# Optimization experiments

Hardware: AMD Instinct MI355X
Metric: run time of the kernel (lower is better)

## Reference

```python
import jax, jax.numpy as jnp
import numpy as np
import math
from itertools import combinations_with_replacement

# ---- module constants (init: d_key=16, d_val=64, p=2, is_causal=True) ----
D_KEY, D_VAL, P = 16, 64, 2
B, H, N = 1, 8, 4096

# M: multisets of size p over d_key indices -> [m, p], m = comb(d_key+p-1, p) = 136
M_NP = np.array(list(combinations_with_replacement(range(D_KEY), P)), dtype=np.int64)

def _n_multiset_perms(row):
    counts = np.bincount(row, minlength=D_KEY)
    denom = 1
    for c in counts:
        denom *= math.factorial(int(c))
    return math.factorial(P) / denom

C_NP = np.array([_n_multiset_perms(r) for r in M_NP], dtype=np.float32)  # [m]
ALPHA = np.float32(1.0 / (math.factorial(P) * D_KEY ** (P / 2)))
M_J = jnp.asarray(M_NP)
C_J = jnp.asarray(C_NP)


def _phi(x):
    # x: [..., d_key] -> polynomial features [..., m] via gather + product over p indices
    return jnp.prod(x[..., M_J], axis=-1)


def setup_inputs() -> dict:
    key = jax.random.key(0)
    kq, kk, kv = jax.random.split(key, 3)
    Q = jax.random.normal(kq, (B, H, N, D_KEY), dtype=jnp.float32)
    K = jax.random.normal(kk, (B, H, N, D_KEY), dtype=jnp.float32)
    V = jax.random.normal(kv, (B, H, N, D_VAL), dtype=jnp.float32)
    return {"Q": Q, "K": K, "V": V, "continue_prev": 0}


def reference(Q, K, V, continue_prev):
    # continue_prev is False (0): fresh sequence, no carried state.
    Phi_Q = _phi(Q)  # [b,h,n,m]
    Phi_K = _phi(K)  # [b,h,n,m]
    # causal accumulation: cumsum over token axis (-3)
    H_S = jnp.cumsum(Phi_K[..., None] * V[..., None, :], axis=-3) * ALPHA  # [b,h,n,m,d_val]
    H_Z = jnp.cumsum(Phi_K[..., None], axis=-3) * ALPHA                    # [b,h,n,m,1]
    S_term = jnp.einsum('m,bhnm,bhnmd->bhnd', C_J, Phi_Q, H_S)  # [b,h,n,d_val]
    Z_term = jnp.einsum('m,bhnm,bhnmd->bhnd', C_J, Phi_Q, H_Z)  # [b,h,n,1]
    return (S_term, Z_term)
```

## Files before the change

### kernel.cpp

```cpp
#include <hip/hip_runtime.h>


#define SEQN 4096
#define NHEAD 8
#define DKEY 16
#define DVAL 64
#define CHUNK 128
#define NCHUNK 32
#define ALPHA 0.03125f

typedef float f32x4 __attribute__((ext_vector_type(4)));
typedef __bf16 bf16x4 __attribute__((ext_vector_type(4)));
typedef __bf16 bf16x8 __attribute__((ext_vector_type(8)));
typedef unsigned long long u64;
typedef u64 u64x2 __attribute__((ext_vector_type(2)));

#define SW512(row, colb) (((row) << 9) + ((colb) ^ (((row) & 7) << 4)))
#define SW256(row, colb) (((row) << 8) + ((colb) ^ (((row) & 7) << 4)))

__device__ inline float bf2f(__bf16 x) {
    unsigned short u = __builtin_bit_cast(unsigned short, x);
    unsigned int v = ((unsigned int)u) << 16;
    return __builtin_bit_cast(float, v);
}

__global__ __launch_bounds__(512, 1)
void p01_state(const float* __restrict__ Kg, const float* __restrict__ Vg,
               const float* __restrict__ Qg, __bf16* __restrict__ G,
               float* __restrict__ Og)
{
    __shared__ __align__(128) unsigned char Vt2[80 * 256];
    __shared__ __align__(128) unsigned char Ktf[16 * 512];
    __shared__ __align__(128) unsigned char Kl[128 * 32];
    const int tid = threadIdx.x;
    const int w = tid >> 6;
    const int lane = tid & 63;
    const int r = lane & 15, g = lane >> 4;
    const int bid = blockIdx.x;
    const int h = bid & 7, c = bid >> 3;
    const int k0 = c * CHUNK;
    const int qb = k0 + 16 * w;

    float qr[16];
    {
        const float* qp = Qg + ((size_t)h * SEQN + qb + r) * DKEY;
        #pragma unroll
        for (int m = 0; m < 4; ++m) {
            const f32x4 v = *(const f32x4*)(qp + 4 * m);
            qr[4 * m + 0] = v[0]; qr[4 * m + 1] = v[1];
            qr[4 * m + 2] = v[2]; qr[4 * m + 3] = v[3];
        }
    }

    {
        const int key = tid >> 2, part = tid & 3;
        const float* kp = Kg + ((size_t)h * SEQN + k0 + key) * DKEY + 4 * part;
        const f32x4 a = *(const f32x4*)kp;
        #pragma unroll
        for (int j = 0; j < 4; ++j)
            *(float*)(Ktf + SW512(4 * part + j, key * 4)) = a[j];
        bf16x4 o;
        #pragma unroll
        for (int j = 0; j < 4; ++j) o[j] = (__bf16)a[j];
        *(bf16x4*)(Kl + key * 32 + ((8 * part) ^ ((key & 1) << 4))) = o;
    }
    {
        const int el = tid & 63;
        const int seg = tid >> 6;
        const float* __restrict__ Vh = Vg + (size_t)h * SEQN * DVAL;
        #pragma unroll
        for (int p = 0; p < 2; ++p) {
            const int tb = 8 * (seg + 8 * p);
            bf16x8 v;
            #pragma unroll
            for (int j = 0; j < 8; ++j)
                v[j] = (__bf16)Vh[(size_t)(k0 + tb + j) * DVAL + el];
            *(bf16x8*)(Vt2 + SW256(el, tb * 2)) = v;
        }
    }
    {
        const int row = 64 + (tid >> 5);
        const int i = tid & 31;
        const u64 val = (row == 64) ? 0x3F803F803F803F80ULL : 0ULL;
        *(u64*)(Vt2 + SW256(row, 8 * i)) = val;
    }
    __syncthreads();

    {
        f32x4 acc[2][5] = {};
        #pragma unroll
        for (int ks = 0; ks < 4; ++ks) {
            const int t0 = 32 * ks + 8 * g;
            bf16x8 af[5];
            #pragma unroll
            for (int et = 0; et < 5; ++et)
                af[et] = *(const bf16x8*)(Vt2 + SW256(16 * et + r, t0 * 2));
            const f32x4 kra = *(const f32x4*)(Ktf + SW512(r, t0 * 4));
            const f32x4 krb = *(const f32x4*)(Ktf + SW512(r, t0 * 4 + 16));
            #pragma unroll
            for (int fa = 0; fa < 2; ++fa) {
                const int ft = 2 * w + fa;
                const f32x4 kfa = *(const f32x4*)(Ktf + SW512(ft, t0 * 4));
                const f32x4 kfb = *(const f32x4*)(Ktf + SW512(ft, t0 * 4 + 16));
                bf16x8 bfrag;
                #pragma unroll
                for (int j = 0; j < 4; ++j) {
                    bfrag[j]     = (__bf16)(kfa[j] * kra[j]);
                    bfrag[4 + j] = (__bf16)(kfb[j] * krb[j]);
                }
                #pragma unroll
                for (int et = 0; et < 5; ++et)
                    acc[fa][et] = __builtin_amdgcn_mfma_f32_16x16x32_bf16(
                        bfrag, af[et], acc[fa][et], 0, 0, 0);
            }
        }
        __bf16* Gc = G + (size_t)(h * NCHUNK + c) * 20480;
        #pragma unroll
        for (int fa = 0; fa < 2; ++fa) {
            const int wfa = 2 * w + fa;
            #pragma unroll
            for (int et = 0; et < 5; ++et) {
                bf16x4 o;
                #pragma unroll
                for (int i = 0; i < 4; ++i) o[i] = (__bf16)acc[fa][et][i];
                *(bf16x4*)&Gc[((wfa * 5 + et) * 64 + lane) * 4] = o;
            }
        }
    }

    float qsel[8];
    #pragma unroll
    for (int j = 0; j < 8; ++j) qsel[j] = (g & 1) ? qr[8 + j] : qr[j];
    bf16x8 qfrag = {};
    if (g < 2) {
        #pragma unroll
        for (int j = 0; j < 8; ++j) qfrag[j] = (__bf16)qsel[j];
    }

    f32x4 oacc[4] = {};
    float zin = 0.f;
    const int qG = qb + r;
    const int smax = w >> 1;
    #pragma unroll
    for (int tl = 0; tl < 2; ++tl) {
        #pragma unroll
        for (int ks = 0; ks < 2; ++ks) {
            const int sidx = 2 * tl + ks;
            if (sidx <= smax) {
                const bool diag = (sidx == smax);
                bf16x8 kf[2];
                #pragma unroll
                for (int uk = 0; uk < 2; ++uk) {
                    bf16x8 f = {};
                    if (g < 2) {
                        const int key = 64 * tl + 32 * ks + 16 * uk + r;
                        f = *(const bf16x8*)(Kl + key * 32 + ((16 * g) ^ ((key & 1) << 4)));
                    }
                    kf[uk] = f;
                }
                const f32x4 zero4 = {};
                f32x4 s[2];
                #pragma unroll
                for (int uk = 0; uk < 2; ++uk)
                    s[uk] = __builtin_amdgcn_mfma_f32_16x16x32_bf16(kf[uk], qfrag, zero4, 0, 0, 0);

                bf16x8 pf;
                float zs = 0.f;
                const int k0g = k0 + 64 * tl + 32 * ks;
                #pragma unroll
                for (int uk = 0; uk < 2; ++uk) {
                    const int kGb = k0g + 16 * uk + 4 * g;
                    #pragma unroll
                    for (int i = 0; i < 4; ++i) {
                        const float sv = s[uk][i];
                        float p = ALPHA * sv * sv;
                        if (diag && (kGb + i > qG)) p = 0.f;
                        zs += p;
                        pf[4 * uk + i] = (__bf16)p;
                    }
                }
                zin += zs;
                #pragma unroll
                for (int dt = 0; dt < 4; ++dt) {
                    const int base = 128 * tl + 64 * ks + 8 * g;
                    u64x2 both;
                    both[0] = *(const u64*)(Vt2 + SW256(16 * dt + r, base));
                    both[1] = *(const u64*)(Vt2 + SW256(16 * dt + r, base + 32));
                    const bf16x8 vf = __builtin_bit_cast(bf16x8, both);
                    oacc[dt] = __builtin_amdgcn_mfma_f32_16x16x32_bf16(vf, pf, oacc[dt], 0, 0, 0);
                }
            }
        }
    }

    const int q = qb + r;
    #pragma unroll
    for (int dt = 0; dt < 4; ++dt) {
        float* op = Og + ((size_t)h * SEQN + q) * DVAL + 16 * dt + 4 * g;
        *(f32x4*)op = oacc[dt];
    }
    zin += __shfl_xor(zin, 16); zin += __shfl_xor(zin, 32);
    if (lane < 16) {
        float* zp = Og + (size_t)NHEAD * SEQN * DVAL + (size_t)h * SEQN + qb;
        zp[r] = zin;
    }
}

__global__ __launch_bounds__(256)
void p2_scan(const __bf16* __restrict__ G, __bf16* __restrict__ Hb)
{
    const int h = blockIdx.x & 7;
    const int fb = blockIdx.x >> 3;
    const int fid = fb * 1024 + 4 * threadIdx.x;
    const __bf16* Gh = G + (size_t)h * NCHUNK * 20480 + fid;
    __bf16* Hh = Hb + (size_t)h * NCHUNK * 20480 + fid;
    f32x4 acc = {};
    #pragma unroll
    for (int cc = 0; cc < NCHUNK; ++cc) {
        bf16x4 o;
        #pragma unroll
        for (int j = 0; j < 4; ++j) o[j] = (__bf16)acc[j];
        *(bf16x4*)&Hh[cc * 20480] = o;
        const bf16x4 v = *(const bf16x4*)&Gh[cc * 20480];
        #pragma unroll
        for (int j = 0; j < 4; ++j) acc[j] += bf2f(v[j]);
    }
}

__global__ __launch_bounds__(256, 2)
void p3s_apply(const float* __restrict__ Qg, const __bf16* __restrict__ Hb,
               float* __restrict__ Og)
{
    __shared__ __align__(128) unsigned char Hlds[80 * 512];
    const int tid = threadIdx.x;
    const int lane = tid & 63;
    const int r = lane & 15, g = lane >> 4;
    const int w = tid >> 6;
    const int bid = blockIdx.x;
    const int h = bid & 7;
    const int x = bid >> 3;
    const int c = x >> 1;
    const int qh = x & 1;
    if (c == 0) return;
    const int qb = c * CHUNK + qh * 64 + 16 * w;
    const int q = qb + r;

    float qr[16];
    {
        const float* qp = Qg + ((size_t)h * SEQN + q) * DKEY;
        #pragma unroll
        for (int m = 0; m < 4; ++m) {
            const f32x4 v = *(const f32x4*)(qp + 4 * m);
            qr[4 * m + 0] = v[0]; qr[4 * m + 1] = v[1];
            qr[4 * m + 2] = v[2]; qr[4 * m + 3] = v[3];
        }
    }
    f32x4 oprev[4];
    #pragma unroll
    for (int dt = 0; dt < 4; ++dt)
        oprev[dt] = *(const f32x4*)(Og + ((size_t)h * SEQN + q) * DVAL + 16 * dt + 4 * g);
    float* zp = Og + (size_t)NHEAD * SEQN * DVAL + (size_t)h * SEQN + qb;
    const float zprev = zp[r];

    {
        const __bf16* Hbc = Hb + (size_t)(h * NCHUNK + c) * 20480;
        #pragma unroll
        for (int k2 = 0; k2 < 10; ++k2) {
            const int U = tid + 256 * k2;
            const int wfa = U / 160;
            const int rem = U - wfa * 160;
            const int et = rem >> 5;
            const int lp = rem & 31;
            const int L0 = 2 * lp, L1 = L0 + 1;
            const int e0 = 16 * et + (L0 & 15), f0 = 16 * wfa + 4 * (L0 >> 4);
            const int e1 = 16 * et + (L1 & 15), f1 = 16 * wfa + 4 * (L1 >> 4);
            const u64x2 v = *(const u64x2*)&Hbc[U * 8];
            *(u64*)(Hlds + SW512(e0, 2 * f0)) = v[0];
            *(u64*)(Hlds + SW512(e1, 2 * f1)) = v[1];
        }
    }
    __syncthreads();

    float qsel[8];
    #pragma unroll
    for (int j = 0; j < 8; ++j) qsel[j] = (g & 1) ? qr[8 + j] : qr[j];
    f32x4 oacc[4] = {};
    f32x4 zacc4 = {};
    #pragma unroll
    for (int ks = 0; ks < 8; ++ks) {
        const int t0 = 32 * ks + 8 * g;
        bf16x8 af[4];
        #pragma unroll
        for (int dt = 0; dt < 4; ++dt)
            af[dt] = *(const bf16x8*)(Hlds + SW512(16 * dt + r, t0 * 2));
        const bf16x8 afz = *(const bf16x8*)(Hlds + SW512(64 + r, t0 * 2));
        const float qi = ALPHA * ((g & 2) ? qr[2 * ks + 1] : qr[2 * ks]);
        bf16x8 pf;
        #pragma unroll
        for (int j = 0; j < 8; ++j) pf[j] = (__bf16)(qi * qsel[j]);
        #pragma unroll
        for (int dt = 0; dt < 4; ++dt)
            oacc[dt] = __builtin_amdgcn_mfma_f32_16x16x32_bf16(af[dt], pf, oacc[dt], 0, 0, 0);
        zacc4 = __builtin_amdgcn_mfma_f32_16x16x32_bf16(afz, pf, zacc4, 0, 0, 0);
    }

    #pragma unroll
    for (int dt = 0; dt < 4; ++dt) {
        float* op = Og + ((size_t)h * SEQN + q) * DVAL + 16 * dt + 4 * g;
        f32x4 o = oprev[dt];
        #pragma unroll
        for (int i = 0; i < 4; ++i) o[i] += oacc[dt][i];
        *(f32x4*)op = o;
    }
    if (lane < 16)
        zp[r] = zprev + zacc4[0];
}

__global__ __launch_bounds__(128, 2)
void taylor_mono(const float* __restrict__ Qg, const float* __restrict__ Kg,
                 const float* __restrict__ Vg, float* __restrict__ Og)
{
    __shared__ __align__(16) __bf16 Kl[64 * 32];
    __shared__ __align__(16) __bf16 Vt[64 * 72];
    typedef __bf16 bf16x2 __attribute__((ext_vector_type(2)));
    const int tid = threadIdx.x;
    const int wv = tid >> 6;
    const int lane = tid & 63;
    const int r = lane & 15, g = lane >> 4;
    const int bid = blockIdx.x;
    const int h = bid & 7;
    const int tt = bid >> 3;
    const int qt = (tt & 1) ? (tt >> 1) : (63 - (tt >> 1));
    const int qb = qt * 64 + wv * 32;
    const float* __restrict__ Qh = Qg + (size_t)h * SEQN * DKEY;
    const float* __restrict__ Kh = Kg + (size_t)h * SEQN * DKEY;
    const float* __restrict__ Vh = Vg + (size_t)h * SEQN * DVAL;
    for (int row = tid; row < 64; row += 128) {
        bf16x8 z = {};
        *(bf16x8*)&Kl[row * 32 + 16] = z;
        *(bf16x8*)&Kl[row * 32 + 24] = z;
    }
    bf16x8 qfrag[2];
    #pragma unroll
    for (int uq = 0; uq < 2; ++uq) {
        bf16x8 f = {};
        if (g < 2) {
            const float* qp = Qh + (size_t)(qb + 16 * uq + r) * DKEY + 8 * g;
            const f32x4 a = *(const f32x4*)qp;
            const f32x4 b = *(const f32x4*)(qp + 4);
            #pragma unroll
            for (int j = 0; j < 4; ++j) { f[j] = (__bf16)a[j]; f[4 + j] = (__bf16)b[j]; }
        }
        qfrag[uq] = f;
    }
    f32x4 oacc[2][4] = {};
    float zacc0 = 0.f, zacc1 = 0.f;
    const int nkt = qt + 1;
    for (int kt = 0; kt < nkt; ++kt) {
        const int k0 = kt * 64;
        {
            const int key = tid >> 1, half = tid & 1;
            const float* kp = Kh + (size_t)(k0 + key) * DKEY + 8 * half;
            const f32x4 a = *(const f32x4*)kp;
            const f32x4 b = *(const f32x4*)(kp + 4);
            bf16x8 kb;
            #pragma unroll
            for (int j = 0; j < 4; ++j) { kb[j] = (__bf16)a[j]; kb[4 + j] = (__bf16)b[j]; }
            *(bf16x8*)&Kl[key * 32 + 8 * half] = kb;
        }
        {
            const int d = tid & 63;
            const int kp2 = (tid >> 6) * 2;
            #pragma unroll
            for (int i = 0; i < 16; ++i) {
                const int kk = i * 4 + kp2;
                const float a0 = Vh[(size_t)(k0 + kk) * DVAL + d];
                const float a1 = Vh[(size_t)(k0 + kk + 1) * DVAL + d];
                const int w32 = kk & 31;
                const int col = (kk & 32) + ((w32 >> 2) & 3) * 8 + ((w32 >> 4) << 2) + (kk & 3);
                bf16x2 p; p[0] = (__bf16)a0; p[1] = (__bf16)a1;
                *(bf16x2*)&Vt[d * 72 + col] = p;
            }
        }
        __syncthreads();
        const bool diag = (kt + 1 == nkt);
        #pragma unroll
        for (int ks = 0; ks < 2; ++ks) {
            if (k0 + 32 * ks < qb + 32) {
                bf16x8 vfrag[4];
                #pragma unroll
                for (int dt = 0; dt < 4; ++dt)
                    vfrag[dt] = *(const bf16x8*)&Vt[(16 * dt + r) * 72 + 32 * ks + 8 * g];
                bf16x8 kfr[2];
                #pragma unroll
                for (int uk = 0; uk < 2; ++uk)
                    kfr[uk] = *(const bf16x8*)&Kl[(32 * ks + 16 * uk + r) * 32 + 8 * g];
                const f32x4 zero4 = {};
                f32x4 s[2][2];
                #pragma unroll
                for (int uq = 0; uq < 2; ++uq)
                    #pragma unroll
                    for (int uk = 0; uk < 2; ++uk)
                        s[uq][uk] = __builtin_amdgcn_mfma_f32_16x16x32_bf16(
                            kfr[uk], qfrag[uq], zero4, 0, 0, 0);
                #pragma unroll
                for (int uq = 0; uq < 2; ++uq) {
                    bf16x8 pf;
                    float zs = 0.f;
                    #pragma unroll
                    for (int uk = 0; uk < 2; ++uk) {
                        const int kGb = k0 + 32 * ks + 16 * uk + 4 * g;
                        const int qG = qb + 16 * uq + r;
                        #pragma unroll
                        for (int i = 0; i < 4; ++i) {
                            const float sv = s[uq][uk][i];
                            float p = 0.03125f * sv * sv;
                            if (diag && (kGb + i > qG)) p = 0.f;
                            zs += p;
                            pf[4 * uk + i] = (__bf16)p;
                        }
                    }
                    if (uq == 0) zacc0 += zs; else zacc1 += zs;
                    #pragma unroll
                    for (int dt = 0; dt < 4; ++dt)
                        oacc[uq][dt] = __builtin_amdgcn_mfma_f32_16x16x32_bf16(
                            vfrag[dt], pf, oacc[uq][dt], 0, 0, 0);
                }
            }
        }
        __syncthreads();
    }
    #pragma unroll
    for (int uq = 0; uq < 2; ++uq) {
        const int q = qb + 16 * uq + r;
        #pragma unroll
        for (int dt = 0; dt < 4; ++dt) {
            float* op = Og + ((size_t)h * SEQN + q) * DVAL + 16 * dt + 4 * g;
            *(f32x4*)op = oacc[uq][dt];
        }
    }
    zacc0 += __shfl_xor(zacc0, 16); zacc0 += __shfl_xor(zacc0, 32);
    zacc1 += __shfl_xor(zacc1, 16); zacc1 += __shfl_xor(zacc1, 32);
    if (lane < 16) {
        float* zp = Og + (size_t)NHEAD * SEQN * DVAL + (size_t)h * SEQN + qb;
        zp[r] = zacc0;
        zp[16 + r] = zacc1;
    }
}

extern "C" void kernel_launch(void* const* d_in, const int* in_sizes, int n_in,
                              void* d_out, int out_size, void* d_ws, size_t ws_size,
                              hipStream_t stream) {
    const float* Q = (const float*)d_in[0];
    const float* K = (const float*)d_in[1];
    const float* V = (const float*)d_in[2];
    float* O = (float*)d_out;

    const size_t G_OFF  = 0;
    const size_t HB_OFF = 10485760;
    const size_t NEED   = 20971520;

    if (ws_size >= NEED) {
        char* ws = (char*)d_ws;
        __bf16* G  = (__bf16*)(ws + G_OFF);
        __bf16* Hb = (__bf16*)(ws + HB_OFF);
        p01_state<<<dim3(256), dim3(512), 0, stream>>>(K, V, Q, G, O);
        p2_scan  <<<dim3(160), dim3(256), 0, stream>>>(G, Hb);
        p3s_apply<<<dim3(512), dim3(256), 0, stream>>>(Q, Hb, O);
    } else {
        taylor_mono<<<dim3(512), dim3(128), 0, stream>>>(Q, K, V, O);
    }
}
```

Measured before the change: 28.40 us.

## Store intra-chunk partials in bf16 workspace and pre-swizzle scan output for LDS

The intra-chunk kernel now writes its partial outputs and normalizers as bf16 to a workspace instead of fp32 into the final output, which cuts write and read traffic. The scan kernel writes the prefix states directly in the swizzled LDS layout, so the apply kernel can copy them with plain contiguous 16-byte loads instead of scattered stores. The apply kernel switches to 512-thread blocks that cover a whole chunk and no longer skips chunk 0, so it now always writes the final output. This rounds the intra-chunk partial sums to bf16, which reduces accuracy.

```diff
diff --git a/kernel.cpp b/kernel.cpp
--- a/kernel.cpp
+++ b/kernel.cpp
@@ -27,7 +27,7 @@
 __global__ __launch_bounds__(512, 1)
 void p01_state(const float* __restrict__ Kg, const float* __restrict__ Vg,
                const float* __restrict__ Qg, __bf16* __restrict__ G,
-               float* __restrict__ Og)
+               __bf16* __restrict__ Op, __bf16* __restrict__ Zp)
 {
     __shared__ __align__(128) unsigned char Vt2[80 * 256];
     __shared__ __align__(128) unsigned char Ktf[16 * 512];
@@ -196,14 +196,14 @@
     const int q = qb + r;
     #pragma unroll
     for (int dt = 0; dt < 4; ++dt) {
-        float* op = Og + ((size_t)h * SEQN + q) * DVAL + 16 * dt + 4 * g;
-        *(f32x4*)op = oacc[dt];
+        bf16x4 o;
+        #pragma unroll
+        for (int i = 0; i < 4; ++i) o[i] = (__bf16)oacc[dt][i];
+        *(bf16x4*)&Op[((size_t)h * SEQN + q) * DVAL + 16 * dt + 4 * g] = o;
     }
     zin += __shfl_xor(zin, 16); zin += __shfl_xor(zin, 32);
-    if (lane < 16) {
-        float* zp = Og + (size_t)NHEAD * SEQN * DVAL + (size_t)h * SEQN + qb;
-        zp[r] = zin;
-    }
+    if (lane < 16)
+        Zp[(size_t)h * SEQN + qb + r] = (__bf16)zin;
 }
 
 __global__ __launch_bounds__(256)
@@ -211,24 +211,33 @@
 {
     const int h = blockIdx.x & 7;
     const int fb = blockIdx.x >> 3;
-    const int fid = fb * 1024 + 4 * threadIdx.x;
+    const int u = fb * 256 + threadIdx.x;
+    const int fid = 4 * u;
+    const int lane = u & 63;
+    const int ftet = u >> 6;
+    const int wfa = ftet / 5;
+    const int et = ftet - 5 * wfa;
+    const int e = 16 * et + (lane & 15);
+    const int f = 16 * wfa + 4 * (lane >> 4);
+    const int img = SW512(e, 2 * f);
     const __bf16* Gh = G + (size_t)h * NCHUNK * 20480 + fid;
-    __bf16* Hh = Hb + (size_t)h * NCHUNK * 20480 + fid;
+    unsigned char* Hh = (unsigned char*)(Hb + (size_t)h * NCHUNK * 20480) + img;
     f32x4 acc = {};
     #pragma unroll
     for (int cc = 0; cc < NCHUNK; ++cc) {
         bf16x4 o;
         #pragma unroll
         for (int j = 0; j < 4; ++j) o[j] = (__bf16)acc[j];
-        *(bf16x4*)&Hh[cc * 20480] = o;
-        const bf16x4 v = *(const bf16x4*)&Gh[cc * 20480];
+        *(u64*)(Hh + (size_t)cc * 40960) = __builtin_bit_cast(u64, o);
+        const bf16x4 v = *(const bf16x4*)&Gh[(size_t)cc * 20480];
         #pragma unroll
         for (int j = 0; j < 4; ++j) acc[j] += bf2f(v[j]);
     }
 }
 
-__global__ __launch_bounds__(256, 2)
+__global__ __launch_bounds__(512, 1)
 void p3s_apply(const float* __restrict__ Qg, const __bf16* __restrict__ Hb,
+               const __bf16* __restrict__ Op, const __bf16* __restrict__ Zp,
                float* __restrict__ Og)
 {
     __shared__ __align__(128) unsigned char Hlds[80 * 512];
@@ -238,11 +247,8 @@
     const int w = tid >> 6;
     const int bid = blockIdx.x;
     const int h = bid & 7;
-    const int x = bid >> 3;
-    const int c = x >> 1;
-    const int qh = x & 1;
-    if (c == 0) return;
-    const int qb = c * CHUNK + qh * 64 + 16 * w;
+    const int c = bid >> 3;
+    const int qb = c * CHUNK + 16 * w;
     const int q = qb + r;
 
     float qr[16];
@@ -255,28 +261,18 @@
             qr[4 * m + 2] = v[2]; qr[4 * m + 3] = v[3];
         }
     }
-    f32x4 oprev[4];
+    bf16x4 opart[4];
     #pragma unroll
     for (int dt = 0; dt < 4; ++dt)
-        oprev[dt] = *(const f32x4*)(Og + ((size_t)h * SEQN + q) * DVAL + 16 * dt + 4 * g);
-    float* zp = Og + (size_t)NHEAD * SEQN * DVAL + (size_t)h * SEQN + qb;
-    const float zprev = zp[r];
-
-    {
-        const __bf16* Hbc = Hb + (size_t)(h * NCHUNK + c) * 20480;
-        #pragma unroll
-        for (int k2 = 0; k2 < 10; ++k2) {
-            const int U = tid + 256 * k2;
-            const int wfa = U / 160;
-            const int rem = U - wfa * 160;
-            const int et = rem >> 5;
-            const int lp = rem & 31;
-            const int L0 = 2 * lp, L1 = L0 + 1;
-            const int e0 = 16 * et + (L0 & 15), f0 = 16 * wfa + 4 * (L0 >> 4);
-            const int e1 = 16 * et + (L1 & 15), f1 = 16 * wfa + 4 * (L1 >> 4);
-            const u64x2 v = *(const u64x2*)&Hbc[U * 8];
-            *(u64*)(Hlds + SW512(e0, 2 * f0)) = v[0];
-            *(u64*)(Hlds + SW512(e1, 2 * f1)) = v[1];
+        opart[dt] = *(const bf16x4*)&Op[((size_t)h * SEQN + q) * DVAL + 16 * dt + 4 * g];
+    const float zprev = bf2f(Zp[(size_t)h * SEQN + qb + r]);
+
+    {
+        const unsigned char* src = (const unsigned char*)(Hb + (size_t)(h * NCHUNK + c) * 20480);
+        #pragma unroll
+        for (int k2 = 0; k2 < 5; ++k2) {
+            const int off = 16 * (tid + 512 * k2);
+            *(u64x2*)(Hlds + off) = *(const u64x2*)(src + off);
         }
     }
     __syncthreads();
@@ -306,14 +302,15 @@
 
     #pragma unroll
     for (int dt = 0; dt < 4; ++dt) {
-        float* op = Og + ((size_t)h * SEQN + q) * DVAL + 16 * dt + 4 * g;
-        f32x4 o = oprev[dt];
-        #pragma unroll
-        for (int i = 0; i < 4; ++i) o[i] += oacc[dt][i];
-        *(f32x4*)op = o;
-    }
-    if (lane < 16)
+        f32x4 o;
+        #pragma unroll
+        for (int i = 0; i < 4; ++i) o[i] = bf2f(opart[dt][i]) + oacc[dt][i];
+        *(f32x4*)(Og + ((size_t)h * SEQN + q) * DVAL + 16 * dt + 4 * g) = o;
+    }
+    if (lane < 16) {
+        float* zp = Og + (size_t)NHEAD * SEQN * DVAL + (size_t)h * SEQN + qb;
         zp[r] = zprev + zacc4[0];
+    }
 }
 
 __global__ __launch_bounds__(128, 2)
@@ -458,15 +455,19 @@
 
     const size_t G_OFF  = 0;
     const size_t HB_OFF = 10485760;
-    const size_t NEED   = 20971520;
+    const size_t OP_OFF = 20971520;
+    const size_t ZP_OFF = 25165824;
+    const size_t NEED   = 25231360;
 
     if (ws_size >= NEED) {
         char* ws = (char*)d_ws;
         __bf16* G  = (__bf16*)(ws + G_OFF);
         __bf16* Hb = (__bf16*)(ws + HB_OFF);
-        p01_state<<<dim3(256), dim3(512), 0, stream>>>(K, V, Q, G, O);
+        __bf16* Op = (__bf16*)(ws + OP_OFF);
+        __bf16* Zp = (__bf16*)(ws + ZP_OFF);
+        p01_state<<<dim3(256), dim3(512), 0, stream>>>(K, V, Q, G, Op, Zp);
         p2_scan  <<<dim3(160), dim3(256), 0, stream>>>(G, Hb);
-        p3s_apply<<<dim3(512), dim3(256), 0, stream>>>(Q, Hb, O);
+        p3s_apply<<<dim3(256), dim3(512), 0, stream>>>(Q, Hb, Op, Zp, O);
     } else {
         taylor_mono<<<dim3(512), dim3(128), 0, stream>>>(Q, K, V, O);
     }
```

Result: slower. 29.80 us (+4.9%).
